# Kernel tuning notes

Measured on AMD Instinct MI355X. Metric: run time of the kernel, lower is better.

## Reference

```python
import jax, jax.numpy as jnp
import numpy as np

N = 100_000      # nodes
E = 3_200_000    # edges (avg degree 32)
F = 16           # irrep feature channels
IR = 4           # (max_l+1)**2 with max_l = 1
DENOM = 32.0     # denominator init kwarg
EPS = 1e-9
INV_S3 = 1.0 / np.sqrt(3.0).astype(np.float32)  # CG norm for 1x1->0
INV_S2 = 1.0 / np.sqrt(2.0).astype(np.float32)  # CG norm for 1x1->1


def setup_inputs() -> dict:
    key = jax.random.key(0)
    k0, k1, k2, k3, k4 = jax.random.split(key, 5)
    positions = jax.random.normal(k0, (N, 3), jnp.float32)
    node_feats = jax.random.normal(k1, (N, F, IR), jnp.float32)
    W = jax.random.normal(k2, (IR, IR), jnp.float32) / np.float32(np.sqrt(IR))
    b = jnp.zeros((IR,), jnp.float32)
    senders = jax.random.randint(k3, (E,), 0, N)
    receivers = jax.random.randint(k4, (E,), 0, N)
    return dict(positions=positions, node_feats=node_feats, W=W, b=b,
                senders=senders, receivers=receivers)


def reference(positions, node_feats, W, b, senders, receivers):
    # --- edge update: SH of normalized relative position, CG tensor product ---
    d = positions[receivers] - positions[senders]               # [E, 3]
    d = d / (jnp.linalg.norm(d, axis=-1, keepdims=True) + EPS)  # unit direction
    # real spherical harmonics up to l=1: sh0 = 1, sh1 = unit direction
    sh1 = d[:, None, :]                                         # [E, 1, 3]

    x = node_feats[senders]                                     # [E, F, 4]
    x0 = x[..., 0:1]                                            # l=0 part [E,F,1]
    x1 = x[..., 1:4]                                            # l=1 part [E,F,3]

    # CG paths with l3 <= max_l = 1:
    #   0x0->0 (identity), 1x1->0 (dot / sqrt3)
    out0 = x0 + jnp.sum(x1 * sh1, axis=-1, keepdims=True) * INV_S3      # [E,F,1]
    #   0x1->1, 1x0->1 (identities), 1x1->1 (cross / sqrt2)
    cross = jnp.cross(x1, jnp.broadcast_to(sh1, x1.shape))
    out1 = x0 * sh1 + x1 + cross * INV_S2                               # [E,F,3]
    tp = jnp.concatenate([out0, out1], axis=-1)                         # [E,F,4]

    # --- node update: segment-sum over receivers, scale, Dense over coeff dim ---
    agg = jax.ops.segment_sum(tp, receivers, num_segments=positions.shape[0])
    agg = agg / DENOM                                                   # [N,F,4]
    return agg @ W + b                                                  # [N,F,4]
```

## Files before the change

kernel.cpp:

```cpp
#include <hip/hip_runtime.h>


#define F_DIM 16
#define BIN_SHIFT 6
#define BIN_NODES (1 << BIN_SHIFT)
#define Q_NODES 16
#define CHUNK 8192
#define CAP_LDS 768
#define MAXBINS 2048
#define CUR_STRIDE 16

__global__ void __launch_bounds__(256) init_kernel(int* __restrict__ binCur,
                                                   int nbins, int cap)
{
    int b = blockIdx.x * blockDim.x + threadIdx.x;
    if (b < nbins) binCur[b * CUR_STRIDE] = b * cap;
}

__global__ void __launch_bounds__(256) pos_pack_kernel(
    const float* __restrict__ pos, float4* __restrict__ posf4, int N)
{
    int n = blockIdx.x * blockDim.x + threadIdx.x;
    if (n >= N) return;
    posf4[n] = make_float4(pos[3*n], pos[3*n+1], pos[3*n+2], 0.f);
}

__global__ void __launch_bounds__(512) build_bins_kernel(
    const int* __restrict__ senders, const int* __restrict__ receivers,
    int* __restrict__ binCur, int* __restrict__ bins,
    int nbins, int cap, int E)
{
    __shared__ int hbase[MAXBINS];
    __shared__ int hrank[MAXBINS];
    int t = threadIdx.x;
    for (int i = t; i < nbins; i += 512) { hbase[i] = 0; hrank[i] = 0; }
    __syncthreads();

    int base = blockIdx.x * CHUNK;
    int end  = base + CHUNK; if (end > E) end = E;

    for (int e = base + t; e < end; e += 512)
        atomicAdd(&hbase[((unsigned)receivers[e]) >> BIN_SHIFT], 1);
    __syncthreads();

    for (int i = t; i < nbins; i += 512) {
        int c = hbase[i];
        hbase[i] = (c > 0) ? atomicAdd(&binCur[i * CUR_STRIDE], c) : 0;
    }
    __syncthreads();

    for (int e = base + t; e < end; e += 512) {
        int r = receivers[e];
        int s = senders[e];
        int bb = r >> BIN_SHIFT;
        int rank = atomicAdd(&hrank[bb], 1);
        int dest = hbase[bb] + rank;
        if (dest < (bb + 1) * cap)
            bins[dest] = (s << BIN_SHIFT) | (r & (BIN_NODES - 1));
    }
}

__device__ __forceinline__ void edge_acc_d(
    float dx, float dy, float dz, const float4& fx,
    float& a0, float& a1, float& a2, float& a3)
{
    const float INV_S3 = 0.5773502691896258f;
    const float INV_S2 = 0.7071067811865476f;
    float dot = fx.y*dx + fx.z*dy + fx.w*dz;
    a0 += fx.x + dot * INV_S3;
    float c0 = fx.z*dz - fx.w*dy;
    float c1 = fx.w*dx - fx.y*dz;
    float c2 = fx.y*dy - fx.z*dx;
    a1 += fx.x*dx + fx.y + c0 * INV_S2;
    a2 += fx.x*dy + fx.z + c1 * INV_S2;
    a3 += fx.x*dz + fx.w + c2 * INV_S2;
}

__global__ void __launch_bounds__(256) bin_gather_kernel(
    const float4* __restrict__ posf4,
    const float* __restrict__ nf,
    const int* __restrict__ bins,
    const int* __restrict__ binCur,
    const float* __restrict__ W,
    const float* __restrict__ Bias,
    float* __restrict__ out,
    int N, int cap)
{
    __shared__ float4 ledge[CAP_LDS];
    __shared__ float4 lpos[Q_NODES];
    __shared__ int lhist[Q_NODES];
    __shared__ int lscan[Q_NODES];
    __shared__ int lstart[Q_NODES];

    int t = threadIdx.x;
    int bin  = blockIdx.x >> 2;
    int quad = blockIdx.x & 3;
    int node0 = (bin << BIN_SHIFT) + quad * Q_NODES;
    int gbase = bin * cap;

    int cnt = binCur[bin * CUR_STRIDE] - gbase;
    if (cnt > cap) cnt = cap;

    if (t < Q_NODES) {
        lhist[t] = 0;
        int n = node0 + t;
        lpos[t] = (n < N) ? posf4[n] : make_float4(0.f, 0.f, 0.f, 0.f);
    }
    __syncthreads();

    for (int j = t; j < cnt; j += 256) {
        int rl = bins[gbase + j] & (BIN_NODES - 1);
        if ((rl >> 4) == quad) atomicAdd(&lhist[rl & (Q_NODES - 1)], 1);
    }
    __syncthreads();

    if (t < Q_NODES) lscan[t] = lhist[t];
    __syncthreads();
    for (int off = 1; off < Q_NODES; off <<= 1) {
        int v = (t < Q_NODES && t >= off) ? lscan[t - off] : 0;
        __syncthreads();
        if (t < Q_NODES) lscan[t] += v;
        __syncthreads();
    }
    if (t < Q_NODES) { lstart[t] = lscan[t] - lhist[t]; lhist[t] = 0; }
    __syncthreads();

    for (int j = t; j < cnt; j += 256) {
        int pk = bins[gbase + j];
        int rl = pk & (BIN_NODES - 1);
        if ((rl >> 4) != quad) continue;
        int rl16 = rl & (Q_NODES - 1);
        int s = pk >> BIN_SHIFT;
        int rank = atomicAdd(&lhist[rl16], 1);
        int dest = lstart[rl16] + rank;
        if (dest >= CAP_LDS) continue;
        float4 ps = posf4[s];
        float4 pr = lpos[rl16];
        float dx = pr.x - ps.x;
        float dy = pr.y - ps.y;
        float dz = pr.z - ps.z;
        float d2 = dx*dx + dy*dy + dz*dz;
        float inv = __builtin_amdgcn_rsqf(fmaxf(d2, 1e-18f));
        float4 rec;
        rec.x = dx * inv;
        rec.y = dy * inv;
        rec.z = dz * inv;
        rec.w = __int_as_float(s);
        ledge[dest] = rec;
    }
    __syncthreads();

    float w[16];
#pragma unroll
    for (int i = 0; i < 16; ++i) w[i] = W[i];
    float b0 = Bias[0], b1 = Bias[1], b2 = Bias[2], b3 = Bias[3];
    const float sc = 1.0f / 32.0f;

    int f = t & 15;
    const float4* nf4 = (const float4*)nf;

    {
        int nl = t >> 4;
        int n = node0 + nl;
        if (n < N) {
            int s0 = lstart[nl];
            int dcnt = lscan[nl] - s0;
            if (dcnt > CAP_LDS - s0) dcnt = CAP_LDS - s0;

            float a0 = 0.f, a1 = 0.f, a2 = 0.f, a3 = 0.f;
            int j = 0;
            for (; j + 4 <= dcnt; j += 4) {
                float4 e0 = ledge[s0 + j + 0];
                float4 e1 = ledge[s0 + j + 1];
                float4 e2 = ledge[s0 + j + 2];
                float4 e3 = ledge[s0 + j + 3];
                int s_0 = __float_as_int(e0.w);
                int s_1 = __float_as_int(e1.w);
                int s_2 = __float_as_int(e2.w);
                int s_3 = __float_as_int(e3.w);
                float4 q0 = nf4[(unsigned)(s_0 * F_DIM + f)];
                float4 q1 = nf4[(unsigned)(s_1 * F_DIM + f)];
                float4 q2 = nf4[(unsigned)(s_2 * F_DIM + f)];
                float4 q3 = nf4[(unsigned)(s_3 * F_DIM + f)];
                edge_acc_d(e0.x, e0.y, e0.z, q0, a0, a1, a2, a3);
                edge_acc_d(e1.x, e1.y, e1.z, q1, a0, a1, a2, a3);
                edge_acc_d(e2.x, e2.y, e2.z, q2, a0, a1, a2, a3);
                edge_acc_d(e3.x, e3.y, e3.z, q3, a0, a1, a2, a3);
            }
            for (; j < dcnt; ++j) {
                float4 e0 = ledge[s0 + j];
                int s = __float_as_int(e0.w);
                float4 q = nf4[(unsigned)(s * F_DIM + f)];
                edge_acc_d(e0.x, e0.y, e0.z, q, a0, a1, a2, a3);
            }

            a0 *= sc; a1 *= sc; a2 *= sc; a3 *= sc;
            float4 o;
            o.x = a0*w[0] + a1*w[4] + a2*w[8]  + a3*w[12] + b0;
            o.y = a0*w[1] + a1*w[5] + a2*w[9]  + a3*w[13] + b1;
            o.z = a0*w[2] + a1*w[6] + a2*w[10] + a3*w[14] + b2;
            o.w = a0*w[3] + a1*w[7] + a2*w[11] + a3*w[15] + b3;
            ((float4*)out)[(size_t)n * F_DIM + f] = o;
        }
    }
}

__global__ void __launch_bounds__(256) hist_kernel(
    const int* __restrict__ receivers, int* __restrict__ deg,
    int* __restrict__ rank, int E)
{
    int e = blockIdx.x * blockDim.x + threadIdx.x;
    if (e >= E) return;
    rank[e] = atomicAdd(&deg[receivers[e]], 1);
}

__global__ void __launch_bounds__(256) alloc_kernel(
    const int* __restrict__ deg, int* __restrict__ start,
    int* __restrict__ cursor, int N)
{
    __shared__ int tmp[256];
    __shared__ int base;
    int t = threadIdx.x;
    int n = blockIdx.x * blockDim.x + t;
    int v = (n < N) ? deg[n] : 0;
    tmp[t] = v;
    __syncthreads();
    for (int off = 1; off < 256; off <<= 1) {
        int x = (t >= off) ? tmp[t - off] : 0;
        __syncthreads();
        tmp[t] += x;
        __syncthreads();
    }
    int incl = tmp[t];
    if (t == 255) base = atomicAdd(cursor, incl);
    __syncthreads();
    if (n < N) start[n] = base + incl - v;
}

__global__ void __launch_bounds__(256) scatter_kernel(
    const int* __restrict__ senders, const int* __restrict__ receivers,
    const int* __restrict__ rank, const int* __restrict__ start,
    int* __restrict__ csr_s, int E)
{
    int e = blockIdx.x * blockDim.x + threadIdx.x;
    if (e >= E) return;
    csr_s[start[receivers[e]] + rank[e]] = senders[e];
}

__global__ void __launch_bounds__(256) gather_kernel(
    const float* __restrict__ pos,
    const float* __restrict__ nf,
    const int* __restrict__ csr_s,
    const int* __restrict__ start,
    const int* __restrict__ deg,
    const float* __restrict__ W,
    const float* __restrict__ b,
    float* __restrict__ out,
    int N)
{
    const float INV_S3 = 0.5773502691896258f;
    const float INV_S2 = 0.7071067811865476f;

    int tid = blockIdx.x * blockDim.x + threadIdx.x;
    int n = tid >> 4;
    if (n >= N) return;
    int f = tid & 15;

    float rx = pos[3*n], ry = pos[3*n+1], rz = pos[3*n+2];
    int s0 = start[n];
    int dcnt = deg[n];
    float a0 = 0.f, a1 = 0.f, a2 = 0.f, a3 = 0.f;
    const float4* nf4 = (const float4*)nf;

    int s = (dcnt > 0) ? csr_s[s0] : 0;
    for (int j = 0; j < dcnt; ++j) {
        int s_next = (j + 1 < dcnt) ? csr_s[s0 + j + 1] : 0;
        float dx = rx - pos[3*s], dy = ry - pos[3*s+1], dz = rz - pos[3*s+2];
        float d2 = dx*dx + dy*dy + dz*dz;
        float inv = __builtin_amdgcn_rsqf(fmaxf(d2, 1e-18f));
        dx *= inv; dy *= inv; dz *= inv;
        float4 x = nf4[(unsigned)(s * F_DIM + f)];
        float x0 = x.x, x1 = x.y, x2 = x.z, x3 = x.w;
        float dot = x1*dx + x2*dy + x3*dz;
        a0 += x0 + dot * INV_S3;
        float c0 = x2*dz - x3*dy, c1 = x3*dx - x1*dz, c2 = x1*dy - x2*dx;
        a1 += x0*dx + x1 + c0 * INV_S2;
        a2 += x0*dy + x2 + c1 * INV_S2;
        a3 += x0*dz + x3 + c2 * INV_S2;
        s = s_next;
    }
    const float sc = 1.0f / 32.0f;
    a0 *= sc; a1 *= sc; a2 *= sc; a3 *= sc;
    float4 o;
    o.x = a0*W[0] + a1*W[4] + a2*W[8]  + a3*W[12] + b[0];
    o.y = a0*W[1] + a1*W[5] + a2*W[9]  + a3*W[13] + b[1];
    o.z = a0*W[2] + a1*W[6] + a2*W[10] + a3*W[14] + b[2];
    o.w = a0*W[3] + a1*W[7] + a2*W[11] + a3*W[15] + b[3];
    ((float4*)out)[tid] = o;
}

extern "C" void kernel_launch(void* const* d_in, const int* in_sizes, int n_in,
                              void* d_out, int out_size, void* d_ws, size_t ws_size,
                              hipStream_t stream)
{
    const float* pos       = (const float*)d_in[0];
    const float* nf        = (const float*)d_in[1];
    const float* W         = (const float*)d_in[2];
    const float* b         = (const float*)d_in[3];
    const int*   senders   = (const int*)d_in[4];
    const int*   receivers = (const int*)d_in[5];

    int N = in_sizes[0] / 3;
    int E = in_sizes[4];
    float* out = (float*)d_out;
    const int blk = 256;

    int nbins = (N + BIN_NODES - 1) >> BIN_SHIFT;
    int cap   = E / nbins + 453;
    size_t need = ((size_t)N * 4 + (size_t)nbins * cap
                   + (size_t)nbins * CUR_STRIDE) * sizeof(float);

    if (nbins <= MAXBINS && ws_size >= need) {
        float4* posf4 = (float4*)d_ws;
        int* binCur = (int*)(posf4 + N);
        int* bins   = binCur + (size_t)nbins * CUR_STRIDE;

        pos_pack_kernel<<<(N + blk - 1) / blk, blk, 0, stream>>>(pos, posf4, N);
        init_kernel<<<(nbins + blk - 1) / blk, blk, 0, stream>>>(binCur, nbins, cap);
        build_bins_kernel<<<(E + CHUNK - 1) / CHUNK, 512, 0, stream>>>(
            senders, receivers, binCur, bins, nbins, cap, E);
        bin_gather_kernel<<<nbins * 4, blk, 0, stream>>>(
            posf4, nf, bins, binCur, W, b, out, N, cap);
    } else {
        int* cursor = (int*)d_ws;
        int* deg    = cursor + 1;
        int* start  = deg + N;
        int* rank   = start + N;
        int* csr_s  = rank + E;

        hipMemsetAsync(cursor, 0, (size_t)(1 + N) * sizeof(int), stream);
        hist_kernel<<<(E + blk - 1) / blk, blk, 0, stream>>>(receivers, deg, rank, E);
        alloc_kernel<<<(N + blk - 1) / blk, blk, 0, stream>>>(deg, start, cursor, N);
        scatter_kernel<<<(E + blk - 1) / blk, blk, 0, stream>>>(
            senders, receivers, rank, start, csr_s, E);
        long total = (long)N * F_DIM;
        gather_kernel<<<(unsigned)((total + blk - 1) / blk), blk, 0, stream>>>(
            pos, nf, csr_s, start, deg, W, b, out, N);
    }
}
```

Measured before the change: 294.2 us.

## Replace receiver binning with atomic CSR build and contiguous per-block gather

Drops the 64-node bin build and the per-quad rescans of the whole bin. Instead it builds a CSR through a global degree histogram, a block scan, and an atomic scatter that turns the start pointers into end pointers. Each 16-node gather block then reads one contiguous CSR segment and finds each edge's local node from a small prefix array. This removes the fourfold redundant bin reads and the LDS histogram passes in the gather. The cost is two rounds of random global atomics over all edges, and the rank array is removed.

```diff
diff --git a/kernel.cpp b/kernel.cpp
--- a/kernel.cpp
+++ b/kernel.cpp
@@ -2,20 +2,8 @@
 
 
 #define F_DIM 16
-#define BIN_SHIFT 6
-#define BIN_NODES (1 << BIN_SHIFT)
-#define Q_NODES 16
-#define CHUNK 8192
+#define GB_NODES 16
 #define CAP_LDS 768
-#define MAXBINS 2048
-#define CUR_STRIDE 16
-
-__global__ void __launch_bounds__(256) init_kernel(int* __restrict__ binCur,
-                                                   int nbins, int cap)
-{
-    int b = blockIdx.x * blockDim.x + threadIdx.x;
-    if (b < nbins) binCur[b * CUR_STRIDE] = b * cap;
-}
 
 __global__ void __launch_bounds__(256) pos_pack_kernel(
     const float* __restrict__ pos, float4* __restrict__ posf4, int N)
@@ -25,39 +13,45 @@
     posf4[n] = make_float4(pos[3*n], pos[3*n+1], pos[3*n+2], 0.f);
 }
 
-__global__ void __launch_bounds__(512) build_bins_kernel(
+__global__ void __launch_bounds__(256) hist_kernel(
+    const int* __restrict__ receivers, int* __restrict__ deg, int E)
+{
+    int e = blockIdx.x * blockDim.x + threadIdx.x;
+    if (e >= E) return;
+    atomicAdd(&deg[receivers[e]], 1);
+}
+
+__global__ void __launch_bounds__(256) alloc_kernel(
+    const int* __restrict__ deg, int* __restrict__ start,
+    int* __restrict__ cursor, int N)
+{
+    __shared__ int tmp[256];
+    __shared__ int base;
+    int t = threadIdx.x;
+    int n = blockIdx.x * blockDim.x + t;
+    int v = (n < N) ? deg[n] : 0;
+    tmp[t] = v;
+    __syncthreads();
+    for (int off = 1; off < 256; off <<= 1) {
+        int x = (t >= off) ? tmp[t - off] : 0;
+        __syncthreads();
+        tmp[t] += x;
+        __syncthreads();
+    }
+    int incl = tmp[t];
+    if (t == 255) base = atomicAdd(cursor, incl);
+    __syncthreads();
+    if (n < N) start[n] = base + incl - v;
+}
+
+__global__ void __launch_bounds__(256) scatter_kernel(
     const int* __restrict__ senders, const int* __restrict__ receivers,
-    int* __restrict__ binCur, int* __restrict__ bins,
-    int nbins, int cap, int E)
-{
-    __shared__ int hbase[MAXBINS];
-    __shared__ int hrank[MAXBINS];
-    int t = threadIdx.x;
-    for (int i = t; i < nbins; i += 512) { hbase[i] = 0; hrank[i] = 0; }
-    __syncthreads();
-
-    int base = blockIdx.x * CHUNK;
-    int end  = base + CHUNK; if (end > E) end = E;
-
-    for (int e = base + t; e < end; e += 512)
-        atomicAdd(&hbase[((unsigned)receivers[e]) >> BIN_SHIFT], 1);
-    __syncthreads();
-
-    for (int i = t; i < nbins; i += 512) {
-        int c = hbase[i];
-        hbase[i] = (c > 0) ? atomicAdd(&binCur[i * CUR_STRIDE], c) : 0;
-    }
-    __syncthreads();
-
-    for (int e = base + t; e < end; e += 512) {
-        int r = receivers[e];
-        int s = senders[e];
-        int bb = r >> BIN_SHIFT;
-        int rank = atomicAdd(&hrank[bb], 1);
-        int dest = hbase[bb] + rank;
-        if (dest < (bb + 1) * cap)
-            bins[dest] = (s << BIN_SHIFT) | (r & (BIN_NODES - 1));
-    }
+    int* __restrict__ start, int* __restrict__ csr_s, int E)
+{
+    int e = blockIdx.x * blockDim.x + threadIdx.x;
+    if (e >= E) return;
+    int dest = atomicAdd(&start[receivers[e]], 1);
+    csr_s[dest] = senders[e];
 }
 
 __device__ __forceinline__ void edge_acc_d(
@@ -79,63 +73,49 @@
 __global__ void __launch_bounds__(256) bin_gather_kernel(
     const float4* __restrict__ posf4,
     const float* __restrict__ nf,
-    const int* __restrict__ bins,
-    const int* __restrict__ binCur,
+    const int* __restrict__ csr_s,
+    const int* __restrict__ endp,
+    const int* __restrict__ deg,
     const float* __restrict__ W,
     const float* __restrict__ Bias,
     float* __restrict__ out,
-    int N, int cap)
+    int N)
 {
     __shared__ float4 ledge[CAP_LDS];
-    __shared__ float4 lpos[Q_NODES];
-    __shared__ int lhist[Q_NODES];
-    __shared__ int lscan[Q_NODES];
-    __shared__ int lstart[Q_NODES];
+    __shared__ float4 lpos[GB_NODES];
+    __shared__ int ldeg[GB_NODES];
+    __shared__ int lb[GB_NODES + 1];
+    __shared__ int lbase;
 
     int t = threadIdx.x;
-    int bin  = blockIdx.x >> 2;
-    int quad = blockIdx.x & 3;
-    int node0 = (bin << BIN_SHIFT) + quad * Q_NODES;
-    int gbase = bin * cap;
-
-    int cnt = binCur[bin * CUR_STRIDE] - gbase;
-    if (cnt > cap) cnt = cap;
-
-    if (t < Q_NODES) {
-        lhist[t] = 0;
+    int node0 = blockIdx.x * GB_NODES;
+
+    if (t < GB_NODES) {
         int n = node0 + t;
+        int dg = (n < N) ? deg[n] : 0;
+        ldeg[t] = dg;
         lpos[t] = (n < N) ? posf4[n] : make_float4(0.f, 0.f, 0.f, 0.f);
-    }
-    __syncthreads();
-
-    for (int j = t; j < cnt; j += 256) {
-        int rl = bins[gbase + j] & (BIN_NODES - 1);
-        if ((rl >> 4) == quad) atomicAdd(&lhist[rl & (Q_NODES - 1)], 1);
-    }
-    __syncthreads();
-
-    if (t < Q_NODES) lscan[t] = lhist[t];
-    __syncthreads();
-    for (int off = 1; off < Q_NODES; off <<= 1) {
-        int v = (t < Q_NODES && t >= off) ? lscan[t - off] : 0;
-        __syncthreads();
-        if (t < Q_NODES) lscan[t] += v;
-        __syncthreads();
-    }
-    if (t < Q_NODES) { lstart[t] = lscan[t] - lhist[t]; lhist[t] = 0; }
-    __syncthreads();
-
-    for (int j = t; j < cnt; j += 256) {
-        int pk = bins[gbase + j];
-        int rl = pk & (BIN_NODES - 1);
-        if ((rl >> 4) != quad) continue;
-        int rl16 = rl & (Q_NODES - 1);
-        int s = pk >> BIN_SHIFT;
-        int rank = atomicAdd(&lhist[rl16], 1);
-        int dest = lstart[rl16] + rank;
-        if (dest >= CAP_LDS) continue;
+        if (t == 0) lbase = endp[node0] - dg;
+    }
+    __syncthreads();
+    if (t == 0) {
+        int run = 0; lb[0] = 0;
+#pragma unroll
+        for (int i = 0; i < GB_NODES; ++i) { run += ldeg[i]; lb[i + 1] = run; }
+    }
+    __syncthreads();
+
+    int cnt = lb[GB_NODES];
+    if (cnt > CAP_LDS) cnt = CAP_LDS;
+    int base = lbase;
+
+    for (int k = t; k < cnt; k += 256) {
+        int s = csr_s[base + k];
+        int nl = 0;
+#pragma unroll
+        for (int i = 1; i < GB_NODES; ++i) nl += (k >= lb[i]);
         float4 ps = posf4[s];
-        float4 pr = lpos[rl16];
+        float4 pr = lpos[nl];
         float dx = pr.x - ps.x;
         float dy = pr.y - ps.y;
         float dz = pr.z - ps.z;
@@ -146,7 +126,7 @@
         rec.y = dy * inv;
         rec.z = dz * inv;
         rec.w = __int_as_float(s);
-        ledge[dest] = rec;
+        ledge[k] = rec;
     }
     __syncthreads();
 
@@ -157,101 +137,57 @@
     const float sc = 1.0f / 32.0f;
 
     int f = t & 15;
+    int nl = t >> 4;
+    int n = node0 + nl;
     const float4* nf4 = (const float4*)nf;
 
-    {
-        int nl = t >> 4;
-        int n = node0 + nl;
-        if (n < N) {
-            int s0 = lstart[nl];
-            int dcnt = lscan[nl] - s0;
-            if (dcnt > CAP_LDS - s0) dcnt = CAP_LDS - s0;
-
-            float a0 = 0.f, a1 = 0.f, a2 = 0.f, a3 = 0.f;
-            int j = 0;
-            for (; j + 4 <= dcnt; j += 4) {
-                float4 e0 = ledge[s0 + j + 0];
-                float4 e1 = ledge[s0 + j + 1];
-                float4 e2 = ledge[s0 + j + 2];
-                float4 e3 = ledge[s0 + j + 3];
-                int s_0 = __float_as_int(e0.w);
-                int s_1 = __float_as_int(e1.w);
-                int s_2 = __float_as_int(e2.w);
-                int s_3 = __float_as_int(e3.w);
-                float4 q0 = nf4[(unsigned)(s_0 * F_DIM + f)];
-                float4 q1 = nf4[(unsigned)(s_1 * F_DIM + f)];
-                float4 q2 = nf4[(unsigned)(s_2 * F_DIM + f)];
-                float4 q3 = nf4[(unsigned)(s_3 * F_DIM + f)];
-                edge_acc_d(e0.x, e0.y, e0.z, q0, a0, a1, a2, a3);
-                edge_acc_d(e1.x, e1.y, e1.z, q1, a0, a1, a2, a3);
-                edge_acc_d(e2.x, e2.y, e2.z, q2, a0, a1, a2, a3);
-                edge_acc_d(e3.x, e3.y, e3.z, q3, a0, a1, a2, a3);
-            }
-            for (; j < dcnt; ++j) {
-                float4 e0 = ledge[s0 + j];
-                int s = __float_as_int(e0.w);
-                float4 q = nf4[(unsigned)(s * F_DIM + f)];
-                edge_acc_d(e0.x, e0.y, e0.z, q, a0, a1, a2, a3);
-            }
-
-            a0 *= sc; a1 *= sc; a2 *= sc; a3 *= sc;
-            float4 o;
-            o.x = a0*w[0] + a1*w[4] + a2*w[8]  + a3*w[12] + b0;
-            o.y = a0*w[1] + a1*w[5] + a2*w[9]  + a3*w[13] + b1;
-            o.z = a0*w[2] + a1*w[6] + a2*w[10] + a3*w[14] + b2;
-            o.w = a0*w[3] + a1*w[7] + a2*w[11] + a3*w[15] + b3;
-            ((float4*)out)[(size_t)n * F_DIM + f] = o;
+    if (n < N) {
+        int s0 = lb[nl];
+        int e1 = lb[nl + 1]; if (e1 > cnt) e1 = cnt;
+        int dcnt = e1 - s0;  if (dcnt < 0) dcnt = 0;
+
+        float a0 = 0.f, a1 = 0.f, a2 = 0.f, a3 = 0.f;
+        int j = 0;
+        for (; j + 4 <= dcnt; j += 4) {
+            float4 e0 = ledge[s0 + j + 0];
+            float4 e1v = ledge[s0 + j + 1];
+            float4 e2 = ledge[s0 + j + 2];
+            float4 e3 = ledge[s0 + j + 3];
+            int s_0 = __float_as_int(e0.w);
+            int s_1 = __float_as_int(e1v.w);
+            int s_2 = __float_as_int(e2.w);
+            int s_3 = __float_as_int(e3.w);
+            float4 q0 = nf4[(unsigned)(s_0 * F_DIM + f)];
+            float4 q1 = nf4[(unsigned)(s_1 * F_DIM + f)];
+            float4 q2 = nf4[(unsigned)(s_2 * F_DIM + f)];
+            float4 q3 = nf4[(unsigned)(s_3 * F_DIM + f)];
+            edge_acc_d(e0.x,  e0.y,  e0.z,  q0, a0, a1, a2, a3);
+            edge_acc_d(e1v.x, e1v.y, e1v.z, q1, a0, a1, a2, a3);
+            edge_acc_d(e2.x,  e2.y,  e2.z,  q2, a0, a1, a2, a3);
+            edge_acc_d(e3.x,  e3.y,  e3.z,  q3, a0, a1, a2, a3);
         }
-    }
-}
-
-__global__ void __launch_bounds__(256) hist_kernel(
-    const int* __restrict__ receivers, int* __restrict__ deg,
-    int* __restrict__ rank, int E)
-{
-    int e = blockIdx.x * blockDim.x + threadIdx.x;
-    if (e >= E) return;
-    rank[e] = atomicAdd(&deg[receivers[e]], 1);
-}
-
-__global__ void __launch_bounds__(256) alloc_kernel(
-    const int* __restrict__ deg, int* __restrict__ start,
-    int* __restrict__ cursor, int N)
-{
-    __shared__ int tmp[256];
-    __shared__ int base;
-    int t = threadIdx.x;
-    int n = blockIdx.x * blockDim.x + t;
-    int v = (n < N) ? deg[n] : 0;
-    tmp[t] = v;
-    __syncthreads();
-    for (int off = 1; off < 256; off <<= 1) {
-        int x = (t >= off) ? tmp[t - off] : 0;
-        __syncthreads();
-        tmp[t] += x;
-        __syncthreads();
-    }
-    int incl = tmp[t];
-    if (t == 255) base = atomicAdd(cursor, incl);
-    __syncthreads();
-    if (n < N) start[n] = base + incl - v;
-}
-
-__global__ void __launch_bounds__(256) scatter_kernel(
-    const int* __restrict__ senders, const int* __restrict__ receivers,
-    const int* __restrict__ rank, const int* __restrict__ start,
-    int* __restrict__ csr_s, int E)
-{
-    int e = blockIdx.x * blockDim.x + threadIdx.x;
-    if (e >= E) return;
-    csr_s[start[receivers[e]] + rank[e]] = senders[e];
+        for (; j < dcnt; ++j) {
+            float4 e0 = ledge[s0 + j];
+            int s = __float_as_int(e0.w);
+            float4 q = nf4[(unsigned)(s * F_DIM + f)];
+            edge_acc_d(e0.x, e0.y, e0.z, q, a0, a1, a2, a3);
+        }
+
+        a0 *= sc; a1 *= sc; a2 *= sc; a3 *= sc;
+        float4 o;
+        o.x = a0*w[0] + a1*w[4] + a2*w[8]  + a3*w[12] + b0;
+        o.y = a0*w[1] + a1*w[5] + a2*w[9]  + a3*w[13] + b1;
+        o.z = a0*w[2] + a1*w[6] + a2*w[10] + a3*w[14] + b2;
+        o.w = a0*w[3] + a1*w[7] + a2*w[11] + a3*w[15] + b3;
+        ((float4*)out)[(size_t)n * F_DIM + f] = o;
+    }
 }
 
 __global__ void __launch_bounds__(256) gather_kernel(
     const float* __restrict__ pos,
     const float* __restrict__ nf,
     const int* __restrict__ csr_s,
-    const int* __restrict__ start,
+    const int* __restrict__ endp,
     const int* __restrict__ deg,
     const float* __restrict__ W,
     const float* __restrict__ b,
@@ -267,27 +203,24 @@
     int f = tid & 15;
 
     float rx = pos[3*n], ry = pos[3*n+1], rz = pos[3*n+2];
-    int s0 = start[n];
     int dcnt = deg[n];
+    int s0 = endp[n] - dcnt;
     float a0 = 0.f, a1 = 0.f, a2 = 0.f, a3 = 0.f;
     const float4* nf4 = (const float4*)nf;
 
-    int s = (dcnt > 0) ? csr_s[s0] : 0;
     for (int j = 0; j < dcnt; ++j) {
-        int s_next = (j + 1 < dcnt) ? csr_s[s0 + j + 1] : 0;
+        int s = csr_s[s0 + j];
         float dx = rx - pos[3*s], dy = ry - pos[3*s+1], dz = rz - pos[3*s+2];
         float d2 = dx*dx + dy*dy + dz*dz;
         float inv = __builtin_amdgcn_rsqf(fmaxf(d2, 1e-18f));
         dx *= inv; dy *= inv; dz *= inv;
         float4 x = nf4[(unsigned)(s * F_DIM + f)];
-        float x0 = x.x, x1 = x.y, x2 = x.z, x3 = x.w;
-        float dot = x1*dx + x2*dy + x3*dz;
-        a0 += x0 + dot * INV_S3;
-        float c0 = x2*dz - x3*dy, c1 = x3*dx - x1*dz, c2 = x1*dy - x2*dx;
-        a1 += x0*dx + x1 + c0 * INV_S2;
-        a2 += x0*dy + x2 + c1 * INV_S2;
-        a3 += x0*dz + x3 + c2 * INV_S2;
-        s = s_next;
+        float dot = x.y*dx + x.z*dy + x.w*dz;
+        a0 += x.x + dot * INV_S3;
+        float c0 = x.z*dz - x.w*dy, c1 = x.w*dx - x.y*dz, c2 = x.y*dy - x.z*dx;
+        a1 += x.x*dx + x.y + c0 * INV_S2;
+        a2 += x.x*dy + x.z + c1 * INV_S2;
+        a3 += x.x*dz + x.w + c2 * INV_S2;
     }
     const float sc = 1.0f / 32.0f;
     a0 *= sc; a1 *= sc; a2 *= sc; a3 *= sc;
@@ -315,34 +248,34 @@
     float* out = (float*)d_out;
     const int blk = 256;
 
-    int nbins = (N + BIN_NODES - 1) >> BIN_SHIFT;
-    int cap   = E / nbins + 453;
-    size_t need = ((size_t)N * 4 + (size_t)nbins * cap
-                   + (size_t)nbins * CUR_STRIDE) * sizeof(float);
-
-    if (nbins <= MAXBINS && ws_size >= need) {
+    size_t need_main = (size_t)N * 16 + ((size_t)1 + 2*(size_t)N + (size_t)E) * 4;
+
+    if (ws_size >= need_main) {
         float4* posf4 = (float4*)d_ws;
-        int* binCur = (int*)(posf4 + N);
-        int* bins   = binCur + (size_t)nbins * CUR_STRIDE;
-
+        int* cursor = (int*)(posf4 + N);
+        int* deg    = cursor + 1;
+        int* start  = deg + N;
+        int* csr_s  = start + N;
+
+        hipMemsetAsync(cursor, 0, (size_t)(1 + N) * sizeof(int), stream);
         pos_pack_kernel<<<(N + blk - 1) / blk, blk, 0, stream>>>(pos, posf4, N);
-        init_kernel<<<(nbins + blk - 1) / blk, blk, 0, stream>>>(binCur, nbins, cap);
-        build_bins_kernel<<<(E + CHUNK - 1) / CHUNK, 512, 0, stream>>>(
-            senders, receivers, binCur, bins, nbins, cap, E);
-        bin_gather_kernel<<<nbins * 4, blk, 0, stream>>>(
-            posf4, nf, bins, binCur, W, b, out, N, cap);
+        hist_kernel<<<(E + blk - 1) / blk, blk, 0, stream>>>(receivers, deg, E);
+        alloc_kernel<<<(N + blk - 1) / blk, blk, 0, stream>>>(deg, start, cursor, N);
+        scatter_kernel<<<(E + blk - 1) / blk, blk, 0, stream>>>(
+            senders, receivers, start, csr_s, E);
+        bin_gather_kernel<<<(N + GB_NODES - 1) / GB_NODES, blk, 0, stream>>>(
+            posf4, nf, csr_s, start, deg, W, b, out, N);
     } else {
         int* cursor = (int*)d_ws;
         int* deg    = cursor + 1;
         int* start  = deg + N;
-        int* rank   = start + N;
-        int* csr_s  = rank + E;
+        int* csr_s  = start + N;
 
         hipMemsetAsync(cursor, 0, (size_t)(1 + N) * sizeof(int), stream);
-        hist_kernel<<<(E + blk - 1) / blk, blk, 0, stream>>>(receivers, deg, rank, E);
+        hist_kernel<<<(E + blk - 1) / blk, blk, 0, stream>>>(receivers, deg, E);
         alloc_kernel<<<(N + blk - 1) / blk, blk, 0, stream>>>(deg, start, cursor, N);
         scatter_kernel<<<(E + blk - 1) / blk, blk, 0, stream>>>(
-            senders, receivers, rank, start, csr_s, E);
+            senders, receivers, start, csr_s, E);
         long total = (long)N * F_DIM;
         gather_kernel<<<(unsigned)((total + blk - 1) / blk), blk, 0, stream>>>(
             pos, nf, csr_s, start, deg, W, b, out, N);
```

New measurement: 620.8 us. +111.0%, slower.
